# Kernel optimization log

Measured on AMD Instinct MI355X. Metric: run time of the kernel, lower is better.

## Reference

```python
import math
import jax, jax.numpy as jnp
import numpy as np


def setup_inputs() -> dict:
    key = jax.random.key(0)
    ks = jax.random.split(key, 11)
    B, L, D = 16, 2048, 1024
    s = 0.02  # weight init scale
    return {
        "queries": jax.random.normal(ks[0], (B, L, D), jnp.float32),
        "keys": jax.random.normal(ks[1], (B, L, D), jnp.float32),
        "values": jax.random.normal(ks[2], (B, L, D), jnp.float32),
        "Wq": jax.random.normal(ks[3], (D, D), jnp.float32) * s,
        "bq": jax.random.normal(ks[4], (D,), jnp.float32) * s,
        "Wk": jax.random.normal(ks[5], (D, D), jnp.float32) * s,
        "bk": jax.random.normal(ks[6], (D,), jnp.float32) * s,
        "Wv": jax.random.normal(ks[7], (D, D), jnp.float32) * s,
        "bv": jax.random.normal(ks[8], (D,), jnp.float32) * s,
        "Wo": jax.random.normal(ks[9], (D, D), jnp.float32) * s,
        "bo": jax.random.normal(ks[10], (D,), jnp.float32) * s,
        "n_heads": 8,
    }


def reference(queries, keys, values, Wq, bq, Wk, bk, Wv, bv, Wo, bo, n_heads):
    B, L, D = queries.shape
    H = n_heads
    E = D // H
    # projections -> (B, H, E, L)
    q = (queries @ Wq.T + bq).reshape(B, L, H, E).transpose(0, 2, 3, 1)
    k = (keys @ Wk.T + bk).reshape(B, L, H, E).transpose(0, 2, 3, 1)
    v = (values @ Wv.T + bv).reshape(B, L, H, E).transpose(0, 2, 3, 1)

    # period-based dependency discovery via FFT cross-correlation
    q_fft = jnp.fft.rfft(q, axis=-1)
    k_fft = jnp.fft.rfft(k, axis=-1)
    corr = jnp.fft.irfft(q_fft * jnp.conj(k_fft), n=L, axis=-1)  # (B,H,E,L)

    # time-delay aggregation (training variant: batch-shared top-k delays)
    top_k = int(1 * math.log(L))  # factor = 1
    mean_value = corr.mean(axis=(1, 2))  # (B, L)
    _, index = jax.lax.top_k(mean_value.mean(axis=0), top_k)  # (top_k,)
    weights = mean_value[:, index]  # (B, top_k)
    tmp_corr = jax.nn.softmax(weights, axis=-1)  # (B, top_k)

    pos = jnp.arange(L)
    agg = jnp.zeros_like(v)
    for i in range(top_k):  # small fixed loop (top_k = 7)
        rolled = jnp.take(v, (pos + index[i]) % L, axis=-1)  # roll(v, -index[i])
        agg = agg + rolled * tmp_corr[:, i][:, None, None, None]

    out = agg.transpose(0, 3, 1, 2).reshape(B, L, D)  # (B,L,H,E) -> (B,L,D)
    return out @ Wo.T + bo
```

## Files before the change

### kernel.cpp

```cpp
#include <hip/hip_runtime.h>

typedef __attribute__((ext_vector_type(8))) short bf16x8;
typedef __attribute__((ext_vector_type(4))) short s16x4;
typedef __attribute__((ext_vector_type(4))) float f32x4;

__device__ __forceinline__ float bf2f(unsigned short u) {
    union { unsigned int u; float f; } x; x.u = ((unsigned int)u) << 16; return x.f;
}
__device__ __forceinline__ unsigned short f2bf(float f) {
    union { float f; unsigned int u; } x; x.f = f;
    unsigned int u = x.u;
    unsigned int r = (u + 0x7fffu + ((u >> 16) & 1u)) >> 16;
    return (unsigned short)r;
}

#define GLDS16(gp, lp)                                                        \
    __builtin_amdgcn_global_load_lds(                                         \
        (const __attribute__((address_space(1))) void*)(gp),                  \
        (__attribute__((address_space(3))) void*)(lp), 16, 0, 0)

template<int OUT_MODE>
__global__ __launch_bounds__(512, 2)
void gemm256(const unsigned short* __restrict__ A, const unsigned short* __restrict__ Bw,
             const float* __restrict__ bias, void* __restrict__ out_) {
    __shared__ __align__(16) unsigned short sA[2][16384];
    __shared__ __align__(16) unsigned short sB[2][16384];

    const int tid  = threadIdx.x;
    const int lane = tid & 63;
    const int w    = tid >> 6;
    const int wr   = w >> 2, wc = w & 3;
    const int fr   = lane & 15, g4 = lane >> 4;

    const int bid = blockIdx.x;
    const int qq  = (int)gridDim.x >> 3;
    const int swz = (bid & 7) * qq + (bid >> 3);
    const int  col0 = (swz & 3) * 256;
    const long row0 = (long)(swz >> 2) * 256;

    const int srow = tid >> 3;
    const int sj   = (tid & 7) ^ (srow & 7);
    const unsigned short* gA = A  + (size_t)(row0 + srow) * 1024 + sj * 8;
    const unsigned short* gB = Bw + (size_t)(col0 + srow) * 1024 + sj * 8;
    const int ldst = w * 1024;

    auto stage = [&](int buf, int t) {
        const unsigned short* a = gA + t * 64;
        const unsigned short* b = gB + t * 64;
        char* dA = (char*)&sA[buf][0];
        char* dB = (char*)&sB[buf][0];
#pragma unroll
        for (int r = 0; r < 4; ++r)
            GLDS16(a + r * 65536, (__attribute__((address_space(3))) char*)(dA + r * 8192 + ldst));
#pragma unroll
        for (int r = 0; r < 4; ++r)
            GLDS16(b + r * 65536, (__attribute__((address_space(3))) char*)(dB + r * 8192 + ldst));
    };

    f32x4 acc[8][4];
#pragma unroll
    for (int m = 0; m < 8; ++m)
#pragma unroll
        for (int n = 0; n < 4; ++n) acc[m][n] = (f32x4){0.f, 0.f, 0.f, 0.f};

    stage(0, 0);
    stage(1, 1);

    const int mskK = (fr & 7) << 4;

    for (int t = 0; t < 16; ++t) {
        if (t < 15) asm volatile("s_waitcnt vmcnt(8)" ::: "memory");
        else        asm volatile("s_waitcnt vmcnt(0)" ::: "memory");
        asm volatile("s_barrier" ::: "memory");
        __builtin_amdgcn_sched_barrier(0);

        const char* la = (const char*)&sA[t & 1][0];
        const char* lb = (const char*)&sB[t & 1][0];

        bf16x8 bF[2][4];
#pragma unroll
        for (int c = 0; c < 2; ++c)
#pragma unroll
            for (int n = 0; n < 4; ++n) {
                const int row = wc * 64 + n * 16 + fr;
                bF[c][n] = *(const bf16x8*)(lb + row * 128 + ((c * 64 + g4 * 16) ^ mskK));
            }
#pragma unroll
        for (int mh = 0; mh < 2; ++mh) {
            bf16x8 aF[2][4];
#pragma unroll
            for (int c = 0; c < 2; ++c)
#pragma unroll
                for (int m = 0; m < 4; ++m) {
                    const int row = wr * 128 + mh * 64 + m * 16 + fr;
                    aF[c][m] = *(const bf16x8*)(la + row * 128 + ((c * 64 + g4 * 16) ^ mskK));
                }
            __builtin_amdgcn_s_setprio(1);
#pragma unroll
            for (int c = 0; c < 2; ++c)
#pragma unroll
                for (int n = 0; n < 4; ++n)
#pragma unroll
                    for (int m = 0; m < 4; ++m)
                        acc[mh * 4 + m][n] =
                            __builtin_amdgcn_mfma_f32_16x16x32_bf16(aF[c][m], bF[c][n], acc[mh * 4 + m][n], 0, 0, 0);
            __builtin_amdgcn_s_setprio(0);
        }

        __builtin_amdgcn_sched_barrier(0);
        asm volatile("s_barrier" ::: "memory");
        if (t + 2 < 16) stage(t & 1, t + 2);
    }

    const int cr = g4 * 4;
    const int cc = fr;
    if constexpr (OUT_MODE == 2) {
        const int b  = (int)(row0 >> 11);
        const int tb = ((int)row0 & 2047) + wr * 128 + cr;
#pragma unroll
        for (int m = 0; m < 8; ++m) {
#pragma unroll
            for (int n = 0; n < 4; ++n) {
                int col = col0 + wc * 64 + n * 16 + cc;
                float bv = bias[col];
                s16x4 o;
#pragma unroll
                for (int j = 0; j < 4; ++j) o[j] = (short)f2bf(acc[m][n][j] + bv);
                *(s16x4*)&((unsigned short*)out_)[((size_t)b * 1024 + col) * 2048 + tb + m * 16] = o;
            }
        }
    } else {
#pragma unroll
        for (int m = 0; m < 8; ++m) {
            long row = row0 + wr * 128 + m * 16 + cr;
#pragma unroll
            for (int n = 0; n < 4; ++n) {
                int col = col0 + wc * 64 + n * 16 + cc;
                float bv = bias[col];
#pragma unroll
                for (int j = 0; j < 4; ++j) {
                    float v = acc[m][n][j] + bv;
                    if constexpr (OUT_MODE == 1) ((float*)out_)[(row + j) * 1024 + col] = v;
                    else ((unsigned short*)out_)[(row + j) * 1024 + col] = f2bf(v);
                }
            }
        }
    }
}

__global__ __launch_bounds__(256)
void cast_f2b(const float* __restrict__ src, unsigned short* __restrict__ dst) {
    const size_t i = ((size_t)blockIdx.x * 256 + threadIdx.x) * 8;
    f32x4 v0 = *(const f32x4*)(src + i);
    f32x4 v1 = *(const f32x4*)(src + i + 4);
    bf16x8 o;
#pragma unroll
    for (int j = 0; j < 4; ++j) o[j] = (short)f2bf(v0[j]);
#pragma unroll
    for (int j = 0; j < 4; ++j) o[4 + j] = (short)f2bf(v1[j]);
    *(bf16x8*)(dst + i) = o;
}

__global__ __launch_bounds__(256)
void cast_wT(const float* __restrict__ src, unsigned short* __restrict__ dst) {
    __shared__ float t[64][65];
    const int bx = blockIdx.x * 64, by = blockIdx.y * 64;
    const int tx = threadIdx.x & 63, ty = threadIdx.x >> 6;
    for (int r = ty; r < 64; r += 4)
        t[r][tx] = src[(size_t)(by + r) * 1024 + bx + tx];
    __syncthreads();
    for (int r = ty; r < 64; r += 4)
        dst[(size_t)(bx + r) * 1024 + by + tx] = f2bf(t[tx][r]);
}

__global__ __launch_bounds__(256)
void bias2_kernel(const float* __restrict__ Wo, const float* __restrict__ bv,
                  const float* __restrict__ bo, float* __restrict__ b2) {
    const int n = blockIdx.x * 4 + (threadIdx.x >> 6);
    const int lane = threadIdx.x & 63;
    float s = 0.f;
    for (int k = lane; k < 1024; k += 64) s += Wo[(size_t)n * 1024 + k] * bv[k];
#pragma unroll
    for (int off = 32; off > 0; off >>= 1) s += __shfl_xor(s, off, 64);
    if (lane == 0) b2[n] = s + bo[n];
}

__device__ __forceinline__ void dft8(float* xr, float* xi) {
    const float c8 = 0.70710678118654752440f;
    float es0r = xr[0] + xr[4], es0i = xi[0] + xi[4];
    float es1r = xr[0] - xr[4], es1i = xi[0] - xi[4];
    float es2r = xr[2] + xr[6], es2i = xi[2] + xi[6];
    float es3r = xr[2] - xr[6], es3i = xi[2] - xi[6];
    float E0r = es0r + es2r, E0i = es0i + es2i;
    float E2r = es0r - es2r, E2i = es0i - es2i;
    float E1r = es1r + es3i, E1i = es1i - es3r;
    float E3r = es1r - es3i, E3i = es1i + es3r;
    float os0r = xr[1] + xr[5], os0i = xi[1] + xi[5];
    float os1r = xr[1] - xr[5], os1i = xi[1] - xi[5];
    float os2r = xr[3] + xr[7], os2i = xi[3] + xi[7];
    float os3r = xr[3] - xr[7], os3i = xi[3] - xi[7];
    float O0r = os0r + os2r, O0i = os0i + os2i;
    float O2r = os0r - os2r, O2i = os0i - os2i;
    float O1r = os1r + os3i, O1i = os1i - os3r;
    float O3r = os1r - os3i, O3i = os1i + os3r;
    float p1 = c8 * (O1r + O1i), q1 = c8 * (O1i - O1r);
    float p3 = c8 * (O3r + O3i), q3 = c8 * (O3i - O3r);
    xr[0] = E0r + O0r; xi[0] = E0i + O0i;
    xr[4] = E0r - O0r; xi[4] = E0i - O0i;
    xr[1] = E1r + p1;  xi[1] = E1i + q1;
    xr[5] = E1r - p1;  xi[5] = E1i - q1;
    xr[2] = E2r + O2i; xi[2] = E2i - O2r;
    xr[6] = E2r - O2i; xi[6] = E2i + O2r;
    xr[3] = E3r + q3;  xi[3] = E3i - p3;
    xr[7] = E3r - q3;  xi[7] = E3i + p3;
}

__device__ __forceinline__ int padc(int p) { return p + (p >> 5); }

#define TWIDDLE2(wr_, wi_)                                                    \
    {                                                                         \
        float cr_ = (wr_), ci_ = (wi_);                                       \
        _Pragma("unroll")                                                     \
        for (int k = 1; k < 8; ++k) {                                         \
            float t0 = ar[k] * cr_ - ai[k] * ci_;                             \
            float t1 = ar[k] * ci_ + ai[k] * cr_;                             \
            ar[k] = t0; ai[k] = t1;                                           \
            float t2 = br[k] * cr_ - bi[k] * ci_;                             \
            float t3 = br[k] * ci_ + bi[k] * cr_;                             \
            br[k] = t2; bi[k] = t3;                                           \
            if (k < 7) {                                                      \
                float nr = cr_ * (wr_) - ci_ * (wi_);                         \
                float ni = cr_ * (wi_) + ci_ * (wr_);                         \
                cr_ = nr; ci_ = ni;                                           \
            }                                                                 \
        }                                                                     \
    }

__global__ __launch_bounds__(256)
void fft_corr(const unsigned short* __restrict__ qt, const unsigned short* __restrict__ kt,
              float* __restrict__ G) {
    __shared__ float2 za[2112];
    __shared__ float2 zb[2112];
    float* zfr0 = (float*)za; float* zfi0 = zfr0 + 2112;
    float* zfr1 = (float*)zb; float* zfi1 = zfr1 + 2112;
    const int tid = threadIdx.x;
    const int b = blockIdx.x >> 7;
    const int chunk = blockIdx.x & 127;

    const float N2PI = -6.28318530717958647692f;
    float w1r, w1i, w2r, w2i, w3r, w3i;
    {
        float s, c;
        __sincosf(N2PI * (float)tid * (1.0f / 2048.0f), &s, &c); w1r = c; w1i = s;
        __sincosf(N2PI * (float)(tid & 31) * (1.0f / 256.0f), &s, &c); w2r = c; w2i = s;
        __sincosf(N2PI * (float)(tid & 3) * (1.0f / 32.0f),  &s, &c); w3r = c; w3i = s;
    }

    float aR0 = 0.f, aI0 = 0.f, aR1 = 0.f, aI1 = 0.f;
    float aR2 = 0.f, aI2 = 0.f, aR3 = 0.f, aI3 = 0.f, aR4 = 0.f;

    const int beta = tid >> 5, s2 = tid & 31;
    const int gam  = tid >> 2, u3 = tid & 3;

    for (int it = 0; it < 4; ++it) {
        const int d0 = chunk * 8 + it * 2;
        const unsigned short* q0 = qt + ((size_t)b * 1024 + d0) * 2048;
        const unsigned short* k0 = kt + ((size_t)b * 1024 + d0) * 2048;
        const unsigned short* q1 = q0 + 2048;
        const unsigned short* k1 = k0 + 2048;

        float ar[8], ai[8], br[8], bi[8];
#pragma unroll
        for (int k = 0; k < 8; ++k) {
            ar[k] = bf2f(q0[tid + 256 * k]); ai[k] = bf2f(k0[tid + 256 * k]);
            br[k] = bf2f(q1[tid + 256 * k]); bi[k] = bf2f(k1[tid + 256 * k]);
        }
        dft8(ar, ai); dft8(br, bi);
        TWIDDLE2(w1r, w1i)
#pragma unroll
        for (int k = 0; k < 8; ++k) {
            const int p = padc(256 * k + tid);
            za[p] = make_float2(ar[k], ai[k]);
            zb[p] = make_float2(br[k], bi[k]);
        }
        __syncthreads();

#pragma unroll
        for (int k = 0; k < 8; ++k) {
            const int p = padc(256 * beta + 32 * k + s2);
            float2 va = za[p]; ar[k] = va.x; ai[k] = va.y;
            float2 vb = zb[p]; br[k] = vb.x; bi[k] = vb.y;
        }
        dft8(ar, ai); dft8(br, bi);
        TWIDDLE2(w2r, w2i)
#pragma unroll
        for (int k = 0; k < 8; ++k) {
            const int p = padc(256 * beta + 32 * k + s2);
            za[p] = make_float2(ar[k], ai[k]);
            zb[p] = make_float2(br[k], bi[k]);
        }
        __syncthreads();

#pragma unroll
        for (int k = 0; k < 8; ++k) {
            const int p = padc(32 * gam + 4 * k + u3);
            float2 va = za[p]; ar[k] = va.x; ai[k] = va.y;
            float2 vb = zb[p]; br[k] = vb.x; bi[k] = vb.y;
        }
        dft8(ar, ai); dft8(br, bi);
        TWIDDLE2(w3r, w3i)
#pragma unroll
        for (int k = 0; k < 8; ++k) {
            const int p = padc(32 * gam + 4 * k + u3);
            za[p] = make_float2(ar[k], ai[k]);
            zb[p] = make_float2(br[k], bi[k]);
        }
        __syncthreads();

#pragma unroll
        for (int k = 0; k < 8; ++k) {
            const int p = padc(8 * tid + k);
            float2 va = za[p]; ar[k] = va.x; ai[k] = va.y;
            float2 vb = zb[p]; br[k] = vb.x; bi[k] = vb.y;
        }
        __syncthreads();

#pragma unroll
        for (int blk = 0; blk < 2; ++blk) {
            const int o = 4 * blk;
            {
                float s0r = ar[o] + ar[o + 2], s0i = ai[o] + ai[o + 2];
                float s1r = ar[o] - ar[o + 2], s1i = ai[o] - ai[o + 2];
                float s2r = ar[o + 1] + ar[o + 3], s2i = ai[o + 1] + ai[o + 3];
                float s3r = ar[o + 1] - ar[o + 3], s3i = ai[o + 1] - ai[o + 3];
                ar[o + 0] = s0r + s2r; ai[o + 0] = s0i + s2i;
                ar[o + 2] = s0r - s2r; ai[o + 2] = s0i - s2i;
                ar[o + 1] = s1r + s3i; ai[o + 1] = s1i - s3r;
                ar[o + 3] = s1r - s3i; ai[o + 3] = s1i + s3r;
            }
            {
                float s0r = br[o] + br[o + 2], s0i = bi[o] + bi[o + 2];
                float s1r = br[o] - br[o + 2], s1i = bi[o] - bi[o + 2];
                float s2r = br[o + 1] + br[o + 3], s2i = bi[o + 1] + bi[o + 3];
                float s3r = br[o + 1] - br[o + 3], s3i = bi[o + 1] - bi[o + 3];
                br[o + 0] = s0r + s2r; bi[o + 0] = s0i + s2i;
                br[o + 2] = s0r - s2r; bi[o + 2] = s0i - s2i;
                br[o + 1] = s1r + s3i; bi[o + 1] = s1i - s3r;
                br[o + 3] = s1r - s3i; bi[o + 3] = s1i + s3r;
            }
        }
        {
            const int k1 = tid >> 5;
            const int k2 = (tid >> 2) & 7;
            const int fb = k1 + 8 * k2;
#pragma unroll
            for (int blk = 0; blk < 2; ++blk) {
                const int k3 = (2 * (tid & 3) + blk) & 7;
#pragma unroll
                for (int k4 = 0; k4 < 4; ++k4) {
                    const int f = fb + 64 * k3 + 512 * k4;
                    const int pf = padc(f);
                    zfr0[pf] = ar[4 * blk + k4]; zfi0[pf] = ai[4 * blk + k4];
                    zfr1[pf] = br[4 * blk + k4]; zfi1[pf] = bi[4 * blk + k4];
                }
            }
        }
        __syncthreads();

#pragma unroll
        for (int k = 0; k < 4; ++k) {
            const int f = tid + 256 * k;
            const int f2 = (2048 - f) & 2047;
            const int pf = padc(f), pf2 = padc(f2);
            float Zr = zfr0[pf],  Zi = zfi0[pf];
            float Yr = zfr0[pf2], Yi = -zfi0[pf2];
            float Qr = 0.5f * (Zr + Yr), Qi = 0.5f * (Zi + Yi);
            float Kr = 0.5f * (Zi - Yi), Ki = -0.5f * (Zr - Yr);
            float dR = Qr * Kr + Qi * Ki;
            float dI = Qi * Kr - Qr * Ki;
            Zr = zfr1[pf];  Zi = zfi1[pf];
            Yr = zfr1[pf2]; Yi = -zfi1[pf2];
            Qr = 0.5f * (Zr + Yr); Qi = 0.5f * (Zi + Yi);
            Kr = 0.5f * (Zi - Yi); Ki = -0.5f * (Zr - Yr);
            dR += Qr * Kr + Qi * Ki;
            dI += Qi * Kr - Qr * Ki;
            if      (k == 0) { aR0 += dR; aI0 += dI; }
            else if (k == 1) { aR1 += dR; aI1 += dI; }
            else if (k == 2) { aR2 += dR; aI2 += dI; }
            else             { aR3 += dR; aI3 += dI; }
        }
        if (tid == 0) {
            const int pf = padc(1024);
            aR4 += zfr0[pf] * zfi0[pf] + zfr1[pf] * zfi1[pf];
        }
        __syncthreads();
    }

    atomicAdd(&G[((size_t)b * 1025 + tid +   0) * 2 + 0], aR0);
    atomicAdd(&G[((size_t)b * 1025 + tid +   0) * 2 + 1], aI0);
    atomicAdd(&G[((size_t)b * 1025 + tid + 256) * 2 + 0], aR1);
    atomicAdd(&G[((size_t)b * 1025 + tid + 256) * 2 + 1], aI1);
    atomicAdd(&G[((size_t)b * 1025 + tid + 512) * 2 + 0], aR2);
    atomicAdd(&G[((size_t)b * 1025 + tid + 512) * 2 + 1], aI2);
    atomicAdd(&G[((size_t)b * 1025 + tid + 768) * 2 + 0], aR3);
    atomicAdd(&G[((size_t)b * 1025 + tid + 768) * 2 + 1], aI3);
    if (tid == 0)
        atomicAdd(&G[((size_t)b * 1025 + 1024) * 2 + 0], aR4);
}

__device__ __forceinline__ void fft2048(float* zr, float* zi,
                                        const float* twr, const float* twi, int tid) {
    for (int t = tid; t < 2048; t += 256) {
        int j = __brev((unsigned)t) >> 21;
        if (j > t) {
            float a = zr[t]; zr[t] = zr[j]; zr[j] = a;
            float c = zi[t]; zi[t] = zi[j]; zi[j] = c;
        }
    }
    __syncthreads();
    for (int s = 0; s < 11; ++s) {
        const int m = 1 << s;
        for (int i = tid; i < 1024; i += 256) {
            const int pos = i & (m - 1);
            const int i1  = ((i >> s) << (s + 1)) + pos;
            const int i2  = i1 + m;
            const int tw  = pos << (10 - s);
            float wr = twr[tw], wi = twi[tw];
            float xr = zr[i2], xi = zi[i2];
            float tr = wr * xr - wi * xi;
            float ti = wr * xi + wi * xr;
            float ur = zr[i1], ui = zi[i1];
            zr[i2] = ur - tr; zi[i2] = ui - ti;
            zr[i1] = ur + tr; zi[i1] = ui + ti;
        }
        __syncthreads();
    }
}

__device__ __forceinline__ void init_twiddle(float* twr, float* twi, int tid) {
    for (int j = tid; j < 1024; j += 256) {
        float ang = -6.28318530717958647692f * (float)j * (1.0f / 2048.0f);
        twr[j] = cosf(ang);
        twi[j] = sinf(ang);
    }
}

__global__ __launch_bounds__(256)
void irfft_mean(const float* __restrict__ G, float* __restrict__ mv) {
    __shared__ float zr[2048], zi[2048];
    __shared__ float twr[1024], twi[1024];
    const int tid = threadIdx.x;
    const int b = blockIdx.x;
    init_twiddle(twr, twi, tid);
    for (int f = tid; f < 2048; f += 256) {
        int g = (f <= 1024) ? f : 2048 - f;
        float gr = G[((size_t)b * 1025 + g) * 2 + 0];
        float gi = G[((size_t)b * 1025 + g) * 2 + 1];
        zr[f] = gr;
        zi[f] = (f <= 1024) ? -gi : gi;
    }
    __syncthreads();
    fft2048(zr, zi, twr, twi, tid);
    const float sc = 1.0f / (2048.0f * 1024.0f);
    for (int t = tid; t < 2048; t += 256) mv[b * 2048 + t] = zr[t] * sc;
}

__global__ __launch_bounds__(256)
void topk_softmax(const float* __restrict__ mv, int* __restrict__ idx_out,
                  float* __restrict__ w_out) {
    __shared__ float cm[2048];
    __shared__ float wv4[4];
    __shared__ int   wi4[4];
    __shared__ int   sel[7];
    const int tid  = threadIdx.x;
    const int lane = tid & 63;
    const int wvid = tid >> 6;

    for (int t = tid; t < 2048; t += 256) {
        float s = 0.f;
        for (int b = 0; b < 16; ++b) s += mv[b * 2048 + t];
        cm[t] = s * (1.0f / 16.0f);
    }
    __syncthreads();

    for (int it = 0; it < 7; ++it) {
        float best = -3.4e38f; int bi = 1 << 30;
#pragma unroll
        for (int q = 0; q < 8; ++q) {
            const int t = tid + q * 256;
            float v = cm[t];
            if (v > best || (v == best && t < bi)) { best = v; bi = t; }
        }
#pragma unroll
        for (int off = 32; off > 0; off >>= 1) {
            float ov = __shfl_xor(best, off, 64);
            int   oi = __shfl_xor(bi,   off, 64);
            if (ov > best || (ov == best && oi < bi)) { best = ov; bi = oi; }
        }
        if (lane == 0) { wv4[wvid] = best; wi4[wvid] = bi; }
        __syncthreads();
        if (tid == 0) {
            float bb = wv4[0]; int bj = wi4[0];
#pragma unroll
            for (int u = 1; u < 4; ++u)
                if (wv4[u] > bb || (wv4[u] == bb && wi4[u] < bj)) { bb = wv4[u]; bj = wi4[u]; }
            sel[it] = bj;
            idx_out[it] = bj;
            cm[bj] = -3.4e38f;
        }
        __syncthreads();
    }

    if (tid < 16) {
        const int b = tid;
        float wv[7]; float mx = -3.4e38f;
#pragma unroll
        for (int i = 0; i < 7; ++i) { wv[i] = mv[b * 2048 + sel[i]]; mx = fmaxf(mx, wv[i]); }
        float s = 0.f;
#pragma unroll
        for (int i = 0; i < 7; ++i) { wv[i] = expf(wv[i] - mx); s += wv[i]; }
        float inv = 1.0f / s;
#pragma unroll
        for (int i = 0; i < 7; ++i) w_out[b * 7 + i] = wv[i] * inv;
    }
}

__global__ __launch_bounds__(256)
void agg_kernel(const unsigned short* __restrict__ vb, const int* __restrict__ idx,
                const float* __restrict__ w, unsigned short* __restrict__ agg) {
    const int b  = blockIdx.y;
    const int t  = blockIdx.x * 2 + (threadIdx.x >> 7);
    const int d8 = (threadIdx.x & 127) * 8;
    float av[8] = {0.f, 0.f, 0.f, 0.f, 0.f, 0.f, 0.f, 0.f};
#pragma unroll
    for (int i = 0; i < 7; ++i) {
        const int srow = (t + idx[i]) & 2047;
        const float wi = w[b * 7 + i];
        bf16x8 v = *(const bf16x8*)&vb[((size_t)b * 2048 + srow) * 1024 + d8];
#pragma unroll
        for (int j = 0; j < 8; ++j) av[j] += wi * bf2f((unsigned short)v[j]);
    }
    bf16x8 o;
#pragma unroll
    for (int j = 0; j < 8; ++j) o[j] = (short)f2bf(av[j]);
    *(bf16x8*)&agg[((size_t)b * 2048 + t) * 1024 + d8] = o;
}

__global__ __launch_bounds__(256)
void cast_w(const float* __restrict__ src, unsigned short* __restrict__ dst) {
    const int i = (blockIdx.x * 256 + threadIdx.x) * 4;
    f32x4 v = *(const f32x4*)(src + i);
    s16x4 o;
#pragma unroll
    for (int j = 0; j < 4; ++j) o[j] = (short)f2bf(v[j]);
    *(s16x4*)(dst + i) = o;
}

__global__ __launch_bounds__(256)
void zero_f32(float* __restrict__ p, int n) {
    const int i = blockIdx.x * 256 + threadIdx.x;
    if (i < n) p[i] = 0.0f;
}

extern "C" void kernel_launch(void* const* d_in, const int* in_sizes, int n_in,
                              void* d_out, int out_size, void* d_ws, size_t ws_size,
                              hipStream_t stream) {
    const float* queries = (const float*)d_in[0];
    const float* keys    = (const float*)d_in[1];
    const float* values  = (const float*)d_in[2];
    const float* Wq = (const float*)d_in[3];  const float* bq = (const float*)d_in[4];
    const float* Wk = (const float*)d_in[5];  const float* bk = (const float*)d_in[6];
    const float* Wv = (const float*)d_in[7];  const float* bv = (const float*)d_in[8];
    const float* Wo = (const float*)d_in[9];  const float* bo = (const float*)d_in[10];
    float* out = (float*)d_out;

    char* ws = (char*)d_ws;
    constexpr size_t SZP = (size_t)32768 * 1024 * 2;
    unsigned short* qt  = (unsigned short*)(ws);
    unsigned short* kt  = (unsigned short*)(ws + SZP);
    unsigned short* vb  = (unsigned short*)(ws + 2 * SZP);
    unsigned short* ab  = (unsigned short*)(ws + 3 * SZP);
    unsigned short* wo  = ab;
    unsigned short* wvT = ab + 1048576;
    unsigned short* wq  = (unsigned short*)(ws + 4 * SZP);
    unsigned short* wk  = wq + 1048576;
    unsigned short* W2  = wq + 2097152;
    char* tail = ws + 4 * SZP + 6291456;
    float* zb1024 = (float*)(tail);
    float* b2     = (float*)(tail + 4096);
    float* G      = (float*)(tail + 8192);
    float* mv     = (float*)(tail + 8192 + 131328);
    int*   idx    = (int*)  (tail + 8192 + 131328 + 131072);
    float* wsm    = (float*)(tail + 8192 + 131328 + 131072 + 64);
    unsigned short* agg = qt;

    cast_w<<<1024, 256, 0, stream>>>(Wq, wq);
    cast_w<<<1024, 256, 0, stream>>>(Wk, wk);
    cast_w<<<1024, 256, 0, stream>>>(Wo, wo);
    cast_wT<<<dim3(16, 16), 256, 0, stream>>>(Wv, wvT);
    zero_f32<<<(32800 + 255) / 256, 256, 0, stream>>>(G, 32800);
    zero_f32<<<4, 256, 0, stream>>>(zb1024, 1024);
    bias2_kernel<<<256, 256, 0, stream>>>(Wo, bv, bo, b2);
    gemm256<0><<<16, 512, 0, stream>>>(wo, wvT, zb1024, W2);

    cast_f2b<<<16384, 256, 0, stream>>>(queries, ab);
    gemm256<2><<<512, 512, 0, stream>>>(ab, wq, bq, qt);
    cast_f2b<<<16384, 256, 0, stream>>>(keys, ab);
    gemm256<2><<<512, 512, 0, stream>>>(ab, wk, bk, kt);
    cast_f2b<<<16384, 256, 0, stream>>>(values, vb);

    fft_corr<<<2048, 256, 0, stream>>>(qt, kt, G);
    irfft_mean<<<16, 256, 0, stream>>>(G, mv);
    topk_softmax<<<1, 256, 0, stream>>>(mv, idx, wsm);
    agg_kernel<<<dim3(1024, 16), 256, 0, stream>>>(vb, idx, wsm, agg);
    gemm256<1><<<512, 512, 0, stream>>>(agg, W2, b2, out);
}
```

Baseline: 597.3 us.

## Fold Wq and Wk into one matrix and skip the query projection GEMM

The lag-mean of the cross-correlation over all channels only needs x^T Wq^T Wk y. The change therefore precomputes M = Wq^T Wk with a small GEMM, projects only the keys through M, and casts and transposes the raw queries directly into the FFT input layout. The biases bq and bk only add a lag-independent per-batch constant, which leaves top-k and softmax unchanged. This removes one full projection GEMM and its cast pass, at the cost of an extra bf16 rounding of M. The FFT shared-memory buffers also move from float2 to split real/imaginary arrays.

After: 569.9 us. 1.05x faster.

```diff
diff --git a/kernel.cpp b/kernel.cpp
--- a/kernel.cpp
+++ b/kernel.cpp
@@ -34,7 +34,7 @@
 
     const int bid = blockIdx.x;
     const int qq  = (int)gridDim.x >> 3;
-    const int swz = (bid & 7) * qq + (bid >> 3);
+    const int swz = qq ? (bid & 7) * qq + (bid >> 3) : bid;
     const int  col0 = (swz & 3) * 256;
     const long row0 = (long)(swz >> 2) * 256;
 
@@ -159,6 +159,22 @@
 #pragma unroll
     for (int j = 0; j < 4; ++j) o[4 + j] = (short)f2bf(v1[j]);
     *(bf16x8*)(dst + i) = o;
+}
+
+__global__ __launch_bounds__(256)
+void cast_tq(const float* __restrict__ src, unsigned short* __restrict__ dst) {
+    __shared__ float t[64][65];
+    const int b  = blockIdx.z;
+    const int t0 = blockIdx.x * 64;
+    const int d0 = blockIdx.y * 64;
+    const int tx = threadIdx.x & 63, ty = threadIdx.x >> 6;
+    const float* s = src + ((size_t)b * 2048 + t0) * 1024 + d0;
+    for (int r = ty; r < 64; r += 4)
+        t[r][tx] = s[(size_t)r * 1024 + tx];
+    __syncthreads();
+    unsigned short* d = dst + ((size_t)b * 1024 + d0) * 2048 + t0;
+    for (int r = ty; r < 64; r += 4)
+        d[(size_t)r * 2048 + tx] = f2bf(t[tx][r]);
 }
 
 __global__ __launch_bounds__(256)
@@ -239,10 +255,7 @@
 __global__ __launch_bounds__(256)
 void fft_corr(const unsigned short* __restrict__ qt, const unsigned short* __restrict__ kt,
               float* __restrict__ G) {
-    __shared__ float2 za[2112];
-    __shared__ float2 zb[2112];
-    float* zfr0 = (float*)za; float* zfi0 = zfr0 + 2112;
-    float* zfr1 = (float*)zb; float* zfi1 = zfr1 + 2112;
+    __shared__ float sar[2112], sai[2112], sbr[2112], sbi[2112];
     const int tid = threadIdx.x;
     const int b = blockIdx.x >> 7;
     const int chunk = blockIdx.x & 127;
@@ -280,48 +293,42 @@
 #pragma unroll
         for (int k = 0; k < 8; ++k) {
             const int p = padc(256 * k + tid);
-            za[p] = make_float2(ar[k], ai[k]);
-            zb[p] = make_float2(br[k], bi[k]);
+            sar[p] = ar[k]; sai[p] = ai[k]; sbr[p] = br[k]; sbi[p] = bi[k];
         }
         __syncthreads();
 
 #pragma unroll
         for (int k = 0; k < 8; ++k) {
             const int p = padc(256 * beta + 32 * k + s2);
-            float2 va = za[p]; ar[k] = va.x; ai[k] = va.y;
-            float2 vb = zb[p]; br[k] = vb.x; bi[k] = vb.y;
+            ar[k] = sar[p]; ai[k] = sai[p]; br[k] = sbr[p]; bi[k] = sbi[p];
         }
         dft8(ar, ai); dft8(br, bi);
         TWIDDLE2(w2r, w2i)
 #pragma unroll
         for (int k = 0; k < 8; ++k) {
             const int p = padc(256 * beta + 32 * k + s2);
-            za[p] = make_float2(ar[k], ai[k]);
-            zb[p] = make_float2(br[k], bi[k]);
+            sar[p] = ar[k]; sai[p] = ai[k]; sbr[p] = br[k]; sbi[p] = bi[k];
         }
         __syncthreads();
 
 #pragma unroll
         for (int k = 0; k < 8; ++k) {
             const int p = padc(32 * gam + 4 * k + u3);
-            float2 va = za[p]; ar[k] = va.x; ai[k] = va.y;
-            float2 vb = zb[p]; br[k] = vb.x; bi[k] = vb.y;
+            ar[k] = sar[p]; ai[k] = sai[p]; br[k] = sbr[p]; bi[k] = sbi[p];
         }
         dft8(ar, ai); dft8(br, bi);
         TWIDDLE2(w3r, w3i)
 #pragma unroll
         for (int k = 0; k < 8; ++k) {
             const int p = padc(32 * gam + 4 * k + u3);
-            za[p] = make_float2(ar[k], ai[k]);
-            zb[p] = make_float2(br[k], bi[k]);
+            sar[p] = ar[k]; sai[p] = ai[k]; sbr[p] = br[k]; sbi[p] = bi[k];
         }
         __syncthreads();
 
 #pragma unroll
         for (int k = 0; k < 8; ++k) {
             const int p = padc(8 * tid + k);
-            float2 va = za[p]; ar[k] = va.x; ai[k] = va.y;
-            float2 vb = zb[p]; br[k] = vb.x; bi[k] = vb.y;
+            ar[k] = sar[p]; ai[k] = sai[p]; br[k] = sbr[p]; bi[k] = sbi[p];
         }
         __syncthreads();
 
@@ -360,8 +367,8 @@
                 for (int k4 = 0; k4 < 4; ++k4) {
                     const int f = fb + 64 * k3 + 512 * k4;
                     const int pf = padc(f);
-                    zfr0[pf] = ar[4 * blk + k4]; zfi0[pf] = ai[4 * blk + k4];
-                    zfr1[pf] = br[4 * blk + k4]; zfi1[pf] = bi[4 * blk + k4];
+                    sar[pf] = ar[4 * blk + k4]; sai[pf] = ai[4 * blk + k4];
+                    sbr[pf] = br[4 * blk + k4]; sbi[pf] = bi[4 * blk + k4];
                 }
             }
         }
@@ -372,14 +379,14 @@
             const int f = tid + 256 * k;
             const int f2 = (2048 - f) & 2047;
             const int pf = padc(f), pf2 = padc(f2);
-            float Zr = zfr0[pf],  Zi = zfi0[pf];
-            float Yr = zfr0[pf2], Yi = -zfi0[pf2];
+            float Zr = sar[pf],  Zi = sai[pf];
+            float Yr = sar[pf2], Yi = -sai[pf2];
             float Qr = 0.5f * (Zr + Yr), Qi = 0.5f * (Zi + Yi);
             float Kr = 0.5f * (Zi - Yi), Ki = -0.5f * (Zr - Yr);
             float dR = Qr * Kr + Qi * Ki;
             float dI = Qi * Kr - Qr * Ki;
-            Zr = zfr1[pf];  Zi = zfi1[pf];
-            Yr = zfr1[pf2]; Yi = -zfi1[pf2];
+            Zr = sbr[pf];  Zi = sbi[pf];
+            Yr = sbr[pf2]; Yi = -sbi[pf2];
             Qr = 0.5f * (Zr + Yr); Qi = 0.5f * (Zi + Yi);
             Kr = 0.5f * (Zi - Yi); Ki = -0.5f * (Zr - Yr);
             dR += Qr * Kr + Qi * Ki;
@@ -391,7 +398,7 @@
         }
         if (tid == 0) {
             const int pf = padc(1024);
-            aR4 += zfr0[pf] * zfi0[pf] + zfr1[pf] * zfi1[pf];
+            aR4 += sar[pf] * sai[pf] + sbr[pf] * sbi[pf];
         }
         __syncthreads();
     }
@@ -582,10 +589,11 @@
     unsigned short* ab  = (unsigned short*)(ws + 3 * SZP);
     unsigned short* wo  = ab;
     unsigned short* wvT = ab + 1048576;
-    unsigned short* wq  = (unsigned short*)(ws + 4 * SZP);
-    unsigned short* wk  = wq + 1048576;
-    unsigned short* W2  = wq + 2097152;
-    char* tail = ws + 4 * SZP + 6291456;
+    unsigned short* wqT = ab + 2097152;
+    unsigned short* wkT = ab + 3145728;
+    unsigned short* W2  = (unsigned short*)(ws + 4 * SZP);
+    unsigned short* M   = W2 + 1048576;
+    char* tail = ws + 4 * SZP + 4194304;
     float* zb1024 = (float*)(tail);
     float* b2     = (float*)(tail + 4096);
     float* G      = (float*)(tail + 8192);
@@ -594,19 +602,19 @@
     float* wsm    = (float*)(tail + 8192 + 131328 + 131072 + 64);
     unsigned short* agg = qt;
 
-    cast_w<<<1024, 256, 0, stream>>>(Wq, wq);
-    cast_w<<<1024, 256, 0, stream>>>(Wk, wk);
     cast_w<<<1024, 256, 0, stream>>>(Wo, wo);
     cast_wT<<<dim3(16, 16), 256, 0, stream>>>(Wv, wvT);
+    cast_wT<<<dim3(16, 16), 256, 0, stream>>>(Wq, wqT);
+    cast_wT<<<dim3(16, 16), 256, 0, stream>>>(Wk, wkT);
     zero_f32<<<(32800 + 255) / 256, 256, 0, stream>>>(G, 32800);
     zero_f32<<<4, 256, 0, stream>>>(zb1024, 1024);
     bias2_kernel<<<256, 256, 0, stream>>>(Wo, bv, bo, b2);
     gemm256<0><<<16, 512, 0, stream>>>(wo, wvT, zb1024, W2);
-
-    cast_f2b<<<16384, 256, 0, stream>>>(queries, ab);
-    gemm256<2><<<512, 512, 0, stream>>>(ab, wq, bq, qt);
+    gemm256<0><<<16, 512, 0, stream>>>(wqT, wkT, zb1024, M);
+
     cast_f2b<<<16384, 256, 0, stream>>>(keys, ab);
-    gemm256<2><<<512, 512, 0, stream>>>(ab, wk, bk, kt);
+    gemm256<2><<<512, 512, 0, stream>>>(ab, M, zb1024, kt);
+    cast_tq<<<dim3(32, 16, 16), 256, 0, stream>>>(queries, qt);
     cast_f2b<<<16384, 256, 0, stream>>>(values, vb);
 
     fft_corr<<<2048, 256, 0, stream>>>(qt, kt, G);
```

## Fold Q projection into K via Wq^T·Wk and read fp32 inputs directly

Applied to the files above, without the earlier changes.

Since the channel-summed cross-correlation only needs q·k, it precomputes M = Wq^T Wk and projects the keys with M. Raw fp32 queries then go straight into the FFT, which removes the Q projection GEMM and the queries cast. The dropped bias terms only add a per-batch constant to the lag scores, and the top-k selection and softmax do not change under that shift. The aggregation reads fp32 values directly instead of a bf16 copy, the FFT shared memory switches from padding to an XOR swizzle, and blocks are reordered. The risk is that the FFT now reads queries with a stride of 1024 floats, which coalesces poorly and reads more bytes.

Result: faster. 561.8 us (-5.9%).

```diff
diff --git a/kernel.cpp b/kernel.cpp
--- a/kernel.cpp
+++ b/kernel.cpp
@@ -34,7 +34,7 @@
 
     const int bid = blockIdx.x;
     const int qq  = (int)gridDim.x >> 3;
-    const int swz = (bid & 7) * qq + (bid >> 3);
+    const int swz = qq ? (bid & 7) * qq + (bid >> 3) : bid;
     const int  col0 = (swz & 3) * 256;
     const long row0 = (long)(swz >> 2) * 256;
 
@@ -215,7 +215,7 @@
     xr[7] = E3r - q3;  xi[7] = E3i + p3;
 }
 
-__device__ __forceinline__ int padc(int p) { return p + (p >> 5); }
+__device__ __forceinline__ int ps(int p) { return p ^ (((p >> 5) & 7) << 2); }
 
 #define TWIDDLE2(wr_, wi_)                                                    \
     {                                                                         \
@@ -237,15 +237,15 @@
     }
 
 __global__ __launch_bounds__(256)
-void fft_corr(const unsigned short* __restrict__ qt, const unsigned short* __restrict__ kt,
+void fft_corr(const float* __restrict__ qf, const unsigned short* __restrict__ kt,
               float* __restrict__ G) {
-    __shared__ float2 za[2112];
-    __shared__ float2 zb[2112];
-    float* zfr0 = (float*)za; float* zfi0 = zfr0 + 2112;
-    float* zfr1 = (float*)zb; float* zfi1 = zfr1 + 2112;
+    __shared__ float2 za[2048];
+    __shared__ float2 zb[2048];
     const int tid = threadIdx.x;
-    const int b = blockIdx.x >> 7;
-    const int chunk = blockIdx.x & 127;
+    const int bid = blockIdx.x;
+    const int swzb = (bid & 7) * 256 + (bid >> 3);
+    const int b = swzb >> 7;
+    const int chunk = swzb & 127;
 
     const float N2PI = -6.28318530717958647692f;
     float w1r, w1i, w2r, w2i, w3r, w3i;
@@ -264,22 +264,23 @@
 
     for (int it = 0; it < 4; ++it) {
         const int d0 = chunk * 8 + it * 2;
-        const unsigned short* q0 = qt + ((size_t)b * 1024 + d0) * 2048;
+        const float* qbase = qf + (size_t)b * 2048 * 1024 + d0;
         const unsigned short* k0 = kt + ((size_t)b * 1024 + d0) * 2048;
-        const unsigned short* q1 = q0 + 2048;
         const unsigned short* k1 = k0 + 2048;
 
         float ar[8], ai[8], br[8], bi[8];
 #pragma unroll
         for (int k = 0; k < 8; ++k) {
-            ar[k] = bf2f(q0[tid + 256 * k]); ai[k] = bf2f(k0[tid + 256 * k]);
-            br[k] = bf2f(q1[tid + 256 * k]); bi[k] = bf2f(k1[tid + 256 * k]);
+            const int t = tid + 256 * k;
+            float2 qv = *(const float2*)(qbase + (size_t)t * 1024);
+            ar[k] = qv.x; br[k] = qv.y;
+            ai[k] = bf2f(k0[t]); bi[k] = bf2f(k1[t]);
         }
         dft8(ar, ai); dft8(br, bi);
         TWIDDLE2(w1r, w1i)
 #pragma unroll
         for (int k = 0; k < 8; ++k) {
-            const int p = padc(256 * k + tid);
+            const int p = ps(256 * k + tid);
             za[p] = make_float2(ar[k], ai[k]);
             zb[p] = make_float2(br[k], bi[k]);
         }
@@ -287,7 +288,7 @@
 
 #pragma unroll
         for (int k = 0; k < 8; ++k) {
-            const int p = padc(256 * beta + 32 * k + s2);
+            const int p = ps(256 * beta + 32 * k + s2);
             float2 va = za[p]; ar[k] = va.x; ai[k] = va.y;
             float2 vb = zb[p]; br[k] = vb.x; bi[k] = vb.y;
         }
@@ -295,7 +296,7 @@
         TWIDDLE2(w2r, w2i)
 #pragma unroll
         for (int k = 0; k < 8; ++k) {
-            const int p = padc(256 * beta + 32 * k + s2);
+            const int p = ps(256 * beta + 32 * k + s2);
             za[p] = make_float2(ar[k], ai[k]);
             zb[p] = make_float2(br[k], bi[k]);
         }
@@ -303,7 +304,7 @@
 
 #pragma unroll
         for (int k = 0; k < 8; ++k) {
-            const int p = padc(32 * gam + 4 * k + u3);
+            const int p = ps(32 * gam + 4 * k + u3);
             float2 va = za[p]; ar[k] = va.x; ai[k] = va.y;
             float2 vb = zb[p]; br[k] = vb.x; bi[k] = vb.y;
         }
@@ -311,7 +312,7 @@
         TWIDDLE2(w3r, w3i)
 #pragma unroll
         for (int k = 0; k < 8; ++k) {
-            const int p = padc(32 * gam + 4 * k + u3);
+            const int p = ps(32 * gam + 4 * k + u3);
             za[p] = make_float2(ar[k], ai[k]);
             zb[p] = make_float2(br[k], bi[k]);
         }
@@ -319,7 +320,7 @@
 
 #pragma unroll
         for (int k = 0; k < 8; ++k) {
-            const int p = padc(8 * tid + k);
+            const int p = ps(8 * tid + k);
             float2 va = za[p]; ar[k] = va.x; ai[k] = va.y;
             float2 vb = zb[p]; br[k] = vb.x; bi[k] = vb.y;
         }
@@ -350,18 +351,18 @@
             }
         }
         {
-            const int k1 = tid >> 5;
-            const int k2 = (tid >> 2) & 7;
-            const int fb = k1 + 8 * k2;
+            const int k1d = tid >> 5;
+            const int k2d = (tid >> 2) & 7;
+            const int fb = k1d + 8 * k2d;
 #pragma unroll
             for (int blk = 0; blk < 2; ++blk) {
-                const int k3 = (2 * (tid & 3) + blk) & 7;
+                const int k3d = (2 * (tid & 3) + blk) & 7;
 #pragma unroll
                 for (int k4 = 0; k4 < 4; ++k4) {
-                    const int f = fb + 64 * k3 + 512 * k4;
-                    const int pf = padc(f);
-                    zfr0[pf] = ar[4 * blk + k4]; zfi0[pf] = ai[4 * blk + k4];
-                    zfr1[pf] = br[4 * blk + k4]; zfi1[pf] = bi[4 * blk + k4];
+                    const int f = fb + 64 * k3d + 512 * k4;
+                    const int pf = ps(f);
+                    za[pf] = make_float2(ar[4 * blk + k4], ai[4 * blk + k4]);
+                    zb[pf] = make_float2(br[4 * blk + k4], bi[4 * blk + k4]);
                 }
             }
         }
@@ -371,17 +372,15 @@
         for (int k = 0; k < 4; ++k) {
             const int f = tid + 256 * k;
             const int f2 = (2048 - f) & 2047;
-            const int pf = padc(f), pf2 = padc(f2);
-            float Zr = zfr0[pf],  Zi = zfi0[pf];
-            float Yr = zfr0[pf2], Yi = -zfi0[pf2];
-            float Qr = 0.5f * (Zr + Yr), Qi = 0.5f * (Zi + Yi);
-            float Kr = 0.5f * (Zi - Yi), Ki = -0.5f * (Zr - Yr);
+            const int pf = ps(f), pf2 = ps(f2);
+            float2 Za = za[pf], Ya = za[pf2];
+            float Qr = 0.5f * (Za.x + Ya.x), Qi = 0.5f * (Za.y - Ya.y);
+            float Kr = 0.5f * (Za.y + Ya.y), Ki = -0.5f * (Za.x - Ya.x);
             float dR = Qr * Kr + Qi * Ki;
             float dI = Qi * Kr - Qr * Ki;
-            Zr = zfr1[pf];  Zi = zfi1[pf];
-            Yr = zfr1[pf2]; Yi = -zfi1[pf2];
-            Qr = 0.5f * (Zr + Yr); Qi = 0.5f * (Zi + Yi);
-            Kr = 0.5f * (Zi - Yi); Ki = -0.5f * (Zr - Yr);
+            float2 Zb = zb[pf], Yb = zb[pf2];
+            Qr = 0.5f * (Zb.x + Yb.x); Qi = 0.5f * (Zb.y - Yb.y);
+            Kr = 0.5f * (Zb.y + Yb.y); Ki = -0.5f * (Zb.x - Yb.x);
             dR += Qr * Kr + Qi * Ki;
             dI += Qi * Kr - Qr * Ki;
             if      (k == 0) { aR0 += dR; aI0 += dI; }
@@ -390,8 +389,8 @@
             else             { aR3 += dR; aI3 += dI; }
         }
         if (tid == 0) {
-            const int pf = padc(1024);
-            aR4 += zfr0[pf] * zfi0[pf] + zfr1[pf] * zfi1[pf];
+            const int pf = ps(1024);
+            aR4 += za[pf].x * za[pf].y + zb[pf].x * zb[pf].y;
         }
         __syncthreads();
     }
@@ -526,7 +525,7 @@
 }
 
 __global__ __launch_bounds__(256)
-void agg_kernel(const unsigned short* __restrict__ vb, const int* __restrict__ idx,
+void agg_kernel(const float* __restrict__ vsrc, const int* __restrict__ idx,
                 const float* __restrict__ w, unsigned short* __restrict__ agg) {
     const int b  = blockIdx.y;
     const int t  = blockIdx.x * 2 + (threadIdx.x >> 7);
@@ -536,9 +535,13 @@
     for (int i = 0; i < 7; ++i) {
         const int srow = (t + idx[i]) & 2047;
         const float wi = w[b * 7 + i];
-        bf16x8 v = *(const bf16x8*)&vb[((size_t)b * 2048 + srow) * 1024 + d8];
-#pragma unroll
-        for (int j = 0; j < 8; ++j) av[j] += wi * bf2f((unsigned short)v[j]);
+        const float* src = vsrc + ((size_t)b * 2048 + srow) * 1024 + d8;
+        f32x4 v0 = *(const f32x4*)src;
+        f32x4 v1 = *(const f32x4*)(src + 4);
+#pragma unroll
+        for (int j = 0; j < 4; ++j) av[j] += wi * v0[j];
+#pragma unroll
+        for (int j = 0; j < 4; ++j) av[4 + j] += wi * v1[j];
     }
     bf16x8 o;
 #pragma unroll
@@ -576,42 +579,39 @@
 
     char* ws = (char*)d_ws;
     constexpr size_t SZP = (size_t)32768 * 1024 * 2;
-    unsigned short* qt  = (unsigned short*)(ws);
+    unsigned short* agg = (unsigned short*)(ws);
     unsigned short* kt  = (unsigned short*)(ws + SZP);
-    unsigned short* vb  = (unsigned short*)(ws + 2 * SZP);
     unsigned short* ab  = (unsigned short*)(ws + 3 * SZP);
     unsigned short* wo  = ab;
     unsigned short* wvT = ab + 1048576;
-    unsigned short* wq  = (unsigned short*)(ws + 4 * SZP);
-    unsigned short* wk  = wq + 1048576;
-    unsigned short* W2  = wq + 2097152;
-    char* tail = ws + 4 * SZP + 6291456;
+    unsigned short* wqT = ab + 2097152;
+    unsigned short* wkT = ab + 3145728;
+    unsigned short* W2  = (unsigned short*)(ws + 4 * SZP);
+    unsigned short* M   = W2 + 1048576;
+    char* tail = ws + 4 * SZP + 4194304;
     float* zb1024 = (float*)(tail);
     float* b2     = (float*)(tail + 4096);
     float* G      = (float*)(tail + 8192);
     float* mv     = (float*)(tail + 8192 + 131328);
     int*   idx    = (int*)  (tail + 8192 + 131328 + 131072);
     float* wsm    = (float*)(tail + 8192 + 131328 + 131072 + 64);
-    unsigned short* agg = qt;
-
-    cast_w<<<1024, 256, 0, stream>>>(Wq, wq);
-    cast_w<<<1024, 256, 0, stream>>>(Wk, wk);
+
     cast_w<<<1024, 256, 0, stream>>>(Wo, wo);
     cast_wT<<<dim3(16, 16), 256, 0, stream>>>(Wv, wvT);
+    cast_wT<<<dim3(16, 16), 256, 0, stream>>>(Wq, wqT);
+    cast_wT<<<dim3(16, 16), 256, 0, stream>>>(Wk, wkT);
     zero_f32<<<(32800 + 255) / 256, 256, 0, stream>>>(G, 32800);
     zero_f32<<<4, 256, 0, stream>>>(zb1024, 1024);
     bias2_kernel<<<256, 256, 0, stream>>>(Wo, bv, bo, b2);
     gemm256<0><<<16, 512, 0, stream>>>(wo, wvT, zb1024, W2);
-
-    cast_f2b<<<16384, 256, 0, stream>>>(queries, ab);
-    gemm256<2><<<512, 512, 0, stream>>>(ab, wq, bq, qt);
+    gemm256<0><<<16, 512, 0, stream>>>(wqT, wkT, zb1024, M);
+
     cast_f2b<<<16384, 256, 0, stream>>>(keys, ab);
-    gemm256<2><<<512, 512, 0, stream>>>(ab, wk, bk, kt);
-    cast_f2b<<<16384, 256, 0, stream>>>(values, vb);
-
-    fft_corr<<<2048, 256, 0, stream>>>(qt, kt, G);
+    gemm256<2><<<512, 512, 0, stream>>>(ab, M, zb1024, kt);
+
+    fft_corr<<<2048, 256, 0, stream>>>(queries, kt, G);
     irfft_mean<<<16, 256, 0, stream>>>(G, mv);
     topk_softmax<<<1, 256, 0, stream>>>(mv, idx, wsm);
-    agg_kernel<<<dim3(1024, 16), 256, 0, stream>>>(vb, idx, wsm, agg);
+    agg_kernel<<<dim3(1024, 16), 256, 0, stream>>>(values, idx, wsm, agg);
     gemm256<1><<<512, 512, 0, stream>>>(agg, W2, b2, out);
 }
```
